# Performance work log

Hardware: AMD Instinct MI355X
Metric: run time of the kernel (lower is better)

## Reference

```python
import jax, jax.numpy as jnp
import numpy as np

B, S, H = 2, 2048, 1024
G, HEADS = 4, 16
HPG = HEADS // G          # heads per group = 4
HD = H // HEADS           # head_dim = 64
DG = H // G               # per-group proj dim = 256
SCALE = 1.0 / np.sqrt(HD)


def setup_inputs() -> dict:
    key = jax.random.key(0)
    ks = jax.random.split(key, 6)
    w = 0.02
    return {
        "hidden_states": jax.random.normal(ks[0], (B, S, H), dtype=jnp.float32),
        "Wq": jax.random.normal(ks[1], (G, DG, H), dtype=jnp.float32) * w,
        "bq": jnp.zeros((G, DG), dtype=jnp.float32),
        "Wk": jax.random.normal(ks[2], (G, DG, H), dtype=jnp.float32) * w,
        "bk": jnp.zeros((G, DG), dtype=jnp.float32),
        "Wv": jax.random.normal(ks[3], (G, DG, H), dtype=jnp.float32) * w,
        "bv": jnp.zeros((G, DG), dtype=jnp.float32),
        "Wo": jax.random.normal(ks[4], (H, H), dtype=jnp.float32) * w,
        "bo": jnp.zeros((H,), dtype=jnp.float32),
    }


def _proj_split(x, W, b):
    # x: [B,S,H], W: [G,DG,H], b: [G,DG] -> [B,G,HPG,S,HD]
    y = jnp.einsum("bsh,gdh->bgsd", x, W) + b[None, :, None, :]
    y = y.reshape(x.shape[0], G, x.shape[1], HPG, HD)
    return jnp.transpose(y, (0, 1, 3, 2, 4))


def reference(hidden_states, Wq, bq, Wk, bk, Wv, bv, Wo, bo):
    q = _proj_split(hidden_states, Wq, bq)  # [B,G,HPG,S,HD]
    k = _proj_split(hidden_states, Wk, bk)
    v = _proj_split(hidden_states, Wv, bv)
    scores = jnp.einsum("bghqd,bghkd->bghqk", q, k) * SCALE
    attn = jax.nn.softmax(scores.astype(jnp.float32), axis=-1).astype(v.dtype)
    ctx = jnp.einsum("bghqk,bghkd->bghqd", attn, v)  # [B,G,HPG,S,HD]
    # merge: heads ordered group-major, matching torch cat over group dim
    ctx = jnp.transpose(ctx, (0, 3, 1, 2, 4)).reshape(hidden_states.shape[0], hidden_states.shape[1], H)
    return jnp.einsum("bsh,oh->bso", ctx, Wo) + bo
```

## Files before the change

### kernel.cpp

```cpp
#include <hip/hip_runtime.h>

typedef __bf16 bf16x8 __attribute__((ext_vector_type(8)));
typedef __bf16 bf16x4 __attribute__((ext_vector_type(4)));
typedef short short4v __attribute__((ext_vector_type(4)));
typedef float f32x4 __attribute__((ext_vector_type(4)));

#define LOG2E 1.4426950408889634f

static __device__ __forceinline__ unsigned short f2bf(float f) {
  union { float f; unsigned int u; } c; c.f = f;
  return (unsigned short)((c.u + 0x7fffu + ((c.u >> 16) & 1u)) >> 16);
}

static __device__ __forceinline__ void gload16(const void* g, void* l) {
  __builtin_amdgcn_global_load_lds(
      (const __attribute__((address_space(1))) void*)g,
      (__attribute__((address_space(3))) void*)l, 16, 0, 0);
}

static __device__ __forceinline__ float expfast(float x) {
#if __has_builtin(__builtin_amdgcn_exp2f)
  return __builtin_amdgcn_exp2f(x * LOG2E);
#else
  return exp2f(x * LOG2E);
#endif
}

#if __has_builtin(__builtin_amdgcn_mfma_f32_16x16x16bf16_1k)
#define MFMA16_FALLBACK 0
static __device__ __forceinline__ f32x4 mfma16(bf16x4 a, bf16x4 b, f32x4 c) {
  return __builtin_amdgcn_mfma_f32_16x16x16bf16_1k(
      __builtin_bit_cast(short4v, a), __builtin_bit_cast(short4v, b), c, 0, 0, 0);
}
#else
#define MFMA16_FALLBACK 1
static __device__ __forceinline__ f32x4 mfma16(bf16x4 a, bf16x4 b, f32x4 c) {
  f32x4 d;
  asm("s_nop 1\n\tv_mfma_f32_16x16x16_bf16 %0, %1, %2, %3"
      : "=v"(d) : "v"(a), "v"(b), "v"(c));
  return d;
}
#endif

__global__ void cvt_all(const float* __restrict__ x,
                        const float* __restrict__ Wq,
                        const float* __restrict__ Wk,
                        const float* __restrict__ Wv,
                        const float* __restrict__ Wo,
                        ushort4* __restrict__ dst) {
  int i = blockIdx.x * 256 + threadIdx.x;
  const float* src;
  int off;
  if (i < 1048576) {
    src = x; off = i;
  } else {
    int t = (i - 1048576) >> 18;
    off = (i - 1048576) & 262143;
    src = (t == 0) ? Wq : (t == 1) ? Wk : (t == 2) ? Wv : Wo;
  }
  float4 f = ((const float4*)src)[off];
  ushort4 o;
  o.x = f2bf(f.x); o.y = f2bf(f.y); o.z = f2bf(f.z); o.w = f2bf(f.w);
  dst[i] = o;
}

__launch_bounds__(256, 2)
__global__ void qkv_gemm(const unsigned short* __restrict__ xb,
                         const unsigned short* __restrict__ wq,
                         const unsigned short* __restrict__ wk,
                         const unsigned short* __restrict__ wv,
                         const float* __restrict__ bq,
                         const float* __restrict__ bk,
                         const float* __restrict__ bv,
                         unsigned short* __restrict__ Qo,
                         unsigned short* __restrict__ Ko,
                         unsigned short* __restrict__ VTo) {
  __shared__ unsigned short As[128 * 32];
  __shared__ unsigned short Bs[128 * 32];
  const int s0 = blockIdx.x * 128;
  const int n0g = blockIdx.y * 128;
  const int qkv = n0g >> 10;
  const int d0 = n0g & 1023;
  const unsigned short* W = (qkv == 0) ? wq : ((qkv == 1) ? wk : wv);
  const float* bias = (qkv == 0) ? bq : ((qkv == 1) ? bk : bv);

  const unsigned short* Aptr; const unsigned short* Bptr;
  int Aoff, Boff;
  if (qkv < 2) { Aptr = W;  Aoff = d0; Bptr = xb; Boff = s0; }
  else         { Aptr = xb; Aoff = s0; Bptr = W;  Boff = d0; }

  const int tid = threadIdx.x;
  const int lane = tid & 63;
  const int wid = tid >> 6;
  const int wm = (wid >> 1) * 64;
  const int wn = (wid & 1) * 64;
  const int lm = lane & 15;
  const int quad = lane >> 4;

  const int c0 = tid, c1 = 256 + tid;
  const int ar0 = c0 >> 2, aj0 = c0 & 3;
  const int ar1 = c1 >> 2, aj1 = c1 & 3;

  f32x4 acc[4][4] = {};

  for (int kk = 0; kk < 1024; kk += 32) {
    gload16(Aptr + (size_t)(Aoff + ar0) * 1024 + kk + aj0 * 8, As + c0 * 8);
    gload16(Aptr + (size_t)(Aoff + ar1) * 1024 + kk + aj1 * 8, As + c1 * 8);
    gload16(Bptr + (size_t)(Boff + ar0) * 1024 + kk + aj0 * 8, Bs + c0 * 8);
    gload16(Bptr + (size_t)(Boff + ar1) * 1024 + kk + aj1 * 8, Bs + c1 * 8);
    __syncthreads();
    bf16x8 af[4], bff[4];
#pragma unroll
    for (int mt = 0; mt < 4; ++mt)
      af[mt] = *(const bf16x8*)(As + (wm + mt * 16 + lm) * 32 + quad * 8);
#pragma unroll
    for (int nt = 0; nt < 4; ++nt)
      bff[nt] = *(const bf16x8*)(Bs + (wn + nt * 16 + lm) * 32 + quad * 8);
#pragma unroll
    for (int mt = 0; mt < 4; ++mt)
#pragma unroll
      for (int nt = 0; nt < 4; ++nt)
        acc[mt][nt] = __builtin_amdgcn_mfma_f32_16x16x32_bf16(
            af[mt], bff[nt], acc[mt][nt], 0, 0, 0);
    __syncthreads();
  }

  if (qkv < 2) {
    unsigned short* OUT = (qkv == 0) ? Qo : Ko;
    const float scale = (qkv == 0) ? 0.125f : 1.0f;
#pragma unroll
    for (int mt = 0; mt < 4; ++mt) {
      const int d = d0 + wm + mt * 16 + quad * 4;
      const int g = d >> 8, hpg = (d >> 6) & 3, hd = d & 63;
      const float4 bb = *(const float4*)(bias + d);
#pragma unroll
      for (int nt = 0; nt < 4; ++nt) {
        const int srow = s0 + wn + nt * 16 + lm;
        const int bidx = srow >> 11, s = srow & 2047;
        const int head = (bidx * 4 + g) * 4 + hpg;
        ushort4 o;
        o.x = f2bf((acc[mt][nt][0] + bb.x) * scale);
        o.y = f2bf((acc[mt][nt][1] + bb.y) * scale);
        o.z = f2bf((acc[mt][nt][2] + bb.z) * scale);
        o.w = f2bf((acc[mt][nt][3] + bb.w) * scale);
        *(ushort4*)(OUT + (size_t)head * 131072 + (size_t)s * 64 + hd) = o;
      }
    }
  } else {
#pragma unroll
    for (int nt = 0; nt < 4; ++nt) {
      const int d = d0 + wn + nt * 16 + lm;
      const int g = d >> 8, hpg = (d >> 6) & 3, hd = d & 63;
      const float bb = bias[d];
#pragma unroll
      for (int mt = 0; mt < 4; ++mt) {
        const int sbase = s0 + wm + mt * 16 + quad * 4;
        const int bidx = sbase >> 11, s = sbase & 2047;
        const int head = (bidx * 4 + g) * 4 + hpg;
        ushort4 o;
        o.x = f2bf(acc[mt][nt][0] + bb);
        o.y = f2bf(acc[mt][nt][1] + bb);
        o.z = f2bf(acc[mt][nt][2] + bb);
        o.w = f2bf(acc[mt][nt][3] + bb);
        *(ushort4*)(VTo + (size_t)head * 131072 + (size_t)hd * 2048 + s) = o;
      }
    }
  }
}

static __device__ __forceinline__ void stage_kv(
    const unsigned short* Kh, const unsigned short* Vh, int kv0,
    unsigned short* ksl, unsigned short* vsl, int tid) {
#pragma unroll
  for (int t = 0; t < 4; ++t) {
    int i = t * 256 + tid;
    int slab = i >> 9, kv = (i >> 2) & 127, tp = i & 3;
    int tc = tp ^ ((kv >> 1) & 3);
    gload16(Kh + (size_t)(kv0 + kv) * 64 + slab * 32 + tc * 8, ksl + (size_t)i * 8);
  }
#pragma unroll
  for (int t = 0; t < 4; ++t) {
    int i = t * 256 + tid;
    int hd = i >> 4, tp = i & 15;
    int tc = tp ^ ((hd >> 1) & 7);
    gload16(Vh + (size_t)hd * 2048 + kv0 + tc * 8, vsl + (size_t)i * 8);
  }
}

__launch_bounds__(256, 2)
__global__ void attn_kernel(const unsigned short* __restrict__ Q,
                            const unsigned short* __restrict__ K,
                            const unsigned short* __restrict__ VT,
                            unsigned short* __restrict__ ctx) {
  __shared__ unsigned short Ks[2][8192];
  __shared__ unsigned short Vs[2][8192];

  const int head = blockIdx.y;
  const int q0 = blockIdx.x * 128;
  const int b = head >> 4;
  const int colbase = (head & 15) * 64;

  const unsigned short* Kh = K + (size_t)head * 131072;
  const unsigned short* Vh = VT + (size_t)head * 131072;

  const int tid = threadIdx.x;
  const int lane = tid & 63;
  const int w = tid >> 6;
  const int lm = lane & 15;
  const int quad = lane >> 4;

  bf16x8 qf[2][2];
#pragma unroll
  for (int nt = 0; nt < 2; ++nt) {
    const size_t qrow = (size_t)(q0 + w * 32 + nt * 16 + lm);
#pragma unroll
    for (int c = 0; c < 2; ++c)
      qf[c][nt] = *(const bf16x8*)(Q + (size_t)head * 131072 + qrow * 64 +
                                   c * 32 + quad * 8);
  }

  stage_kv(Kh, Vh, 0, Ks[0], Vs[0], tid);
  __syncthreads();

  float psum[2] = {0.f, 0.f};
  f32x4 oacc[4][2] = {};
  const int kchunk = (quad ^ ((lm >> 1) & 3)) * 8;

  for (int it = 0; it < 16; ++it) {
    const int buf = it & 1;
    if (it < 15)
      stage_kv(Kh, Vh, (it + 1) * 128, Ks[buf ^ 1], Vs[buf ^ 1], tid);

    const unsigned short* kb = Ks[buf];
    const unsigned short* vb = Vs[buf];

#pragma unroll
    for (int mt = 0; mt < 8; ++mt) {
      f32x4 s0 = {}, s1 = {};
#pragma unroll
      for (int c = 0; c < 2; ++c) {
        bf16x8 kf = *(const bf16x8*)(kb + c * 4096 + (mt * 16 + lm) * 32 + kchunk);
        s0 = __builtin_amdgcn_mfma_f32_16x16x32_bf16(kf, qf[c][0], s0, 0, 0, 0);
        s1 = __builtin_amdgcn_mfma_f32_16x16x32_bf16(kf, qf[c][1], s1, 0, 0, 0);
      }
      bf16x4 pf[2];
#pragma unroll
      for (int nt = 0; nt < 2; ++nt) {
        const f32x4 s = nt ? s1 : s0;
        float e0 = expfast(s[0]), e1 = expfast(s[1]);
        float e2 = expfast(s[2]), e3 = expfast(s[3]);
        psum[nt] += (e0 + e1) + (e2 + e3);
        bf16x4 t;
        t[0] = (__bf16)e0; t[1] = (__bf16)e1; t[2] = (__bf16)e2; t[3] = (__bf16)e3;
        pf[nt] = t;
      }
#pragma unroll
      for (int hm = 0; hm < 4; ++hm) {
        bf16x4 vf = *(const bf16x4*)(vb + (hm * 16 + lm) * 128 +
                                     (((mt * 4 + quad) ^ (lm & 14)) * 4));
        oacc[hm][0] = mfma16(vf, pf[0], oacc[hm][0]);
        oacc[hm][1] = mfma16(vf, pf[1], oacc[hm][1]);
      }
    }
    __syncthreads();
  }

#if MFMA16_FALLBACK
  asm volatile("s_nop 7\n\ts_nop 7");
#endif
#pragma unroll
  for (int nt = 0; nt < 2; ++nt) {
    float p = psum[nt];
    p += __shfl_xor(p, 16, 64);
    p += __shfl_xor(p, 32, 64);
    const float inv = 1.0f / p;
    const size_t row = (size_t)(b * 2048 + q0 + w * 32 + nt * 16 + lm);
#pragma unroll
    for (int hm = 0; hm < 4; ++hm) {
      ushort4 o;
      o.x = f2bf(oacc[hm][nt][0] * inv);
      o.y = f2bf(oacc[hm][nt][1] * inv);
      o.z = f2bf(oacc[hm][nt][2] * inv);
      o.w = f2bf(oacc[hm][nt][3] * inv);
      *(ushort4*)(ctx + row * 1024 + colbase + hm * 16 + quad * 4) = o;
    }
  }
}

__launch_bounds__(256, 2)
__global__ void out_gemm(const unsigned short* __restrict__ A,
                         const unsigned short* __restrict__ Wb,
                         const float* __restrict__ bo,
                         float* __restrict__ out) {
  __shared__ unsigned short As[128 * 32];
  __shared__ unsigned short Bs[128 * 32];
  const int s0 = blockIdx.x * 128;
  const int o0 = blockIdx.y * 128;

  const int tid = threadIdx.x;
  const int lane = tid & 63;
  const int wid = tid >> 6;
  const int wm = (wid >> 1) * 64;
  const int wn = (wid & 1) * 64;
  const int lm = lane & 15;
  const int quad = lane >> 4;

  const int c0 = tid, c1 = 256 + tid;
  const int ar0 = c0 >> 2, aj0 = c0 & 3;
  const int ar1 = c1 >> 2, aj1 = c1 & 3;

  f32x4 acc[4][4] = {};

  for (int kk = 0; kk < 1024; kk += 32) {
    gload16(Wb + (size_t)(o0 + ar0) * 1024 + kk + aj0 * 8, As + c0 * 8);
    gload16(Wb + (size_t)(o0 + ar1) * 1024 + kk + aj1 * 8, As + c1 * 8);
    gload16(A + (size_t)(s0 + ar0) * 1024 + kk + aj0 * 8, Bs + c0 * 8);
    gload16(A + (size_t)(s0 + ar1) * 1024 + kk + aj1 * 8, Bs + c1 * 8);
    __syncthreads();
    bf16x8 af[4], bff[4];
#pragma unroll
    for (int mt = 0; mt < 4; ++mt)
      af[mt] = *(const bf16x8*)(As + (wm + mt * 16 + lm) * 32 + quad * 8);
#pragma unroll
    for (int nt = 0; nt < 4; ++nt)
      bff[nt] = *(const bf16x8*)(Bs + (wn + nt * 16 + lm) * 32 + quad * 8);
#pragma unroll
    for (int mt = 0; mt < 4; ++mt)
#pragma unroll
      for (int nt = 0; nt < 4; ++nt)
        acc[mt][nt] = __builtin_amdgcn_mfma_f32_16x16x32_bf16(
            af[mt], bff[nt], acc[mt][nt], 0, 0, 0);
    __syncthreads();
  }

#pragma unroll
  for (int mt = 0; mt < 4; ++mt) {
    const int o = o0 + wm + mt * 16 + quad * 4;
    const float4 bb = *(const float4*)(bo + o);
#pragma unroll
    for (int nt = 0; nt < 4; ++nt) {
      const int s = s0 + wn + nt * 16 + lm;
      float4 v;
      v.x = acc[mt][nt][0] + bb.x;
      v.y = acc[mt][nt][1] + bb.y;
      v.z = acc[mt][nt][2] + bb.z;
      v.w = acc[mt][nt][3] + bb.w;
      *(float4*)(out + (size_t)s * 1024 + o) = v;
    }
  }
}

extern "C" void kernel_launch(void* const* d_in, const int* in_sizes, int n_in,
                              void* d_out, int out_size, void* d_ws, size_t ws_size,
                              hipStream_t stream) {
  const float* x  = (const float*)d_in[0];
  const float* Wq = (const float*)d_in[1];
  const float* bq = (const float*)d_in[2];
  const float* Wk = (const float*)d_in[3];
  const float* bk = (const float*)d_in[4];
  const float* Wv = (const float*)d_in[5];
  const float* bv = (const float*)d_in[6];
  const float* Wo = (const float*)d_in[7];
  const float* bo = (const float*)d_in[8];
  float* out = (float*)d_out;

  char* ws = (char*)d_ws;
  unsigned short* xb  = (unsigned short*)(ws + 0);
  unsigned short* wqb = (unsigned short*)(ws + 8388608);
  unsigned short* wkb = (unsigned short*)(ws + 10485760);
  unsigned short* wvb = (unsigned short*)(ws + 12582912);
  unsigned short* wob = (unsigned short*)(ws + 14680064);
  unsigned short* Qb  = (unsigned short*)(ws + 16777216);
  unsigned short* Kb  = (unsigned short*)(ws + 25165824);
  unsigned short* VTb = (unsigned short*)(ws + 33554432);
  unsigned short* ctxb= (unsigned short*)(ws + 41943040);
  if (ws_size < 50331648) return;

  cvt_all<<<8192, 256, 0, stream>>>(x, Wq, Wk, Wv, Wo, (ushort4*)ws);
  qkv_gemm<<<dim3(32, 24), 256, 0, stream>>>(xb, wqb, wkb, wvb, bq, bk, bv,
                                             Qb, Kb, VTb);
  attn_kernel<<<dim3(16, 32), 256, 0, stream>>>(Qb, Kb, VTb, ctxb);
  out_gemm<<<dim3(32, 8), 256, 0, stream>>>(ctxb, wob, bo, out);
}
```

Before: 198.5 us.

## Deepen GEMM K-tile to 64 with XOR-swizzled LDS and smaller out_gemm tiles

Both projection GEMMs now stage a 64-wide K slice per iteration instead of 32, which halves the number of barrier pairs. Shared-memory rows are XOR-swizzled by row index so the 128-byte rows avoid LDS bank conflicts on the MFMA fragment reads. The output GEMM switches to 128x64 tiles with a doubled grid and launch bounds raised to 4 blocks per CU, to fill more CUs (the old grid had only 256 blocks). The cost is more LDS per block and lower per-block reuse in out_gemm.

```diff
diff --git a/kernel.cpp b/kernel.cpp
--- a/kernel.cpp
+++ b/kernel.cpp
@@ -75,8 +75,8 @@
                          unsigned short* __restrict__ Qo,
                          unsigned short* __restrict__ Ko,
                          unsigned short* __restrict__ VTo) {
-  __shared__ unsigned short As[128 * 32];
-  __shared__ unsigned short Bs[128 * 32];
+  __shared__ unsigned short As[128 * 64];
+  __shared__ unsigned short Bs[128 * 64];
   const int s0 = blockIdx.x * 128;
   const int n0g = blockIdx.y * 128;
   const int qkv = n0g >> 10;
@@ -97,31 +97,40 @@
   const int lm = lane & 15;
   const int quad = lane >> 4;
 
-  const int c0 = tid, c1 = 256 + tid;
-  const int ar0 = c0 >> 2, aj0 = c0 & 3;
-  const int ar1 = c1 >> 2, aj1 = c1 & 3;
-
   f32x4 acc[4][4] = {};
 
-  for (int kk = 0; kk < 1024; kk += 32) {
-    gload16(Aptr + (size_t)(Aoff + ar0) * 1024 + kk + aj0 * 8, As + c0 * 8);
-    gload16(Aptr + (size_t)(Aoff + ar1) * 1024 + kk + aj1 * 8, As + c1 * 8);
-    gload16(Bptr + (size_t)(Boff + ar0) * 1024 + kk + aj0 * 8, Bs + c0 * 8);
-    gload16(Bptr + (size_t)(Boff + ar1) * 1024 + kk + aj1 * 8, Bs + c1 * 8);
+  for (int kk = 0; kk < 1024; kk += 64) {
+#pragma unroll
+    for (int t = 0; t < 4; ++t) {
+      int i = t * 256 + tid;
+      int row = i >> 3, tp = i & 7;
+      int seg = tp ^ (row & 7);
+      gload16(Aptr + (size_t)(Aoff + row) * 1024 + kk + seg * 8,
+              As + (size_t)i * 8);
+      gload16(Bptr + (size_t)(Boff + row) * 1024 + kk + seg * 8,
+              Bs + (size_t)i * 8);
+    }
     __syncthreads();
-    bf16x8 af[4], bff[4];
-#pragma unroll
-    for (int mt = 0; mt < 4; ++mt)
-      af[mt] = *(const bf16x8*)(As + (wm + mt * 16 + lm) * 32 + quad * 8);
-#pragma unroll
-    for (int nt = 0; nt < 4; ++nt)
-      bff[nt] = *(const bf16x8*)(Bs + (wn + nt * 16 + lm) * 32 + quad * 8);
-#pragma unroll
-    for (int mt = 0; mt < 4; ++mt)
-#pragma unroll
-      for (int nt = 0; nt < 4; ++nt)
-        acc[mt][nt] = __builtin_amdgcn_mfma_f32_16x16x32_bf16(
-            af[mt], bff[nt], acc[mt][nt], 0, 0, 0);
+#pragma unroll
+    for (int h = 0; h < 2; ++h) {
+      bf16x8 af[4], bff[4];
+#pragma unroll
+      for (int mt = 0; mt < 4; ++mt) {
+        int r = wm + mt * 16 + lm;
+        af[mt] = *(const bf16x8*)(As + r * 64 + (((h * 4 + quad) ^ (r & 7)) * 8));
+      }
+#pragma unroll
+      for (int nt = 0; nt < 4; ++nt) {
+        int r = wn + nt * 16 + lm;
+        bff[nt] = *(const bf16x8*)(Bs + r * 64 + (((h * 4 + quad) ^ (r & 7)) * 8));
+      }
+#pragma unroll
+      for (int mt = 0; mt < 4; ++mt)
+#pragma unroll
+        for (int nt = 0; nt < 4; ++nt)
+          acc[mt][nt] = __builtin_amdgcn_mfma_f32_16x16x32_bf16(
+              af[mt], bff[nt], acc[mt][nt], 0, 0, 0);
+    }
     __syncthreads();
   }
 
@@ -287,49 +296,62 @@
   }
 }
 
-__launch_bounds__(256, 2)
+__launch_bounds__(256, 4)
 __global__ void out_gemm(const unsigned short* __restrict__ A,
                          const unsigned short* __restrict__ Wb,
                          const float* __restrict__ bo,
                          float* __restrict__ out) {
-  __shared__ unsigned short As[128 * 32];
-  __shared__ unsigned short Bs[128 * 32];
-  const int s0 = blockIdx.x * 128;
+  __shared__ unsigned short As[128 * 64];
+  __shared__ unsigned short Bs[64 * 64];
+  const int s0 = blockIdx.x * 64;
   const int o0 = blockIdx.y * 128;
 
   const int tid = threadIdx.x;
   const int lane = tid & 63;
   const int wid = tid >> 6;
   const int wm = (wid >> 1) * 64;
-  const int wn = (wid & 1) * 64;
+  const int wn = (wid & 1) * 32;
   const int lm = lane & 15;
   const int quad = lane >> 4;
 
-  const int c0 = tid, c1 = 256 + tid;
-  const int ar0 = c0 >> 2, aj0 = c0 & 3;
-  const int ar1 = c1 >> 2, aj1 = c1 & 3;
-
-  f32x4 acc[4][4] = {};
-
-  for (int kk = 0; kk < 1024; kk += 32) {
-    gload16(Wb + (size_t)(o0 + ar0) * 1024 + kk + aj0 * 8, As + c0 * 8);
-    gload16(Wb + (size_t)(o0 + ar1) * 1024 + kk + aj1 * 8, As + c1 * 8);
-    gload16(A + (size_t)(s0 + ar0) * 1024 + kk + aj0 * 8, Bs + c0 * 8);
-    gload16(A + (size_t)(s0 + ar1) * 1024 + kk + aj1 * 8, Bs + c1 * 8);
+  f32x4 acc[4][2] = {};
+
+  for (int kk = 0; kk < 1024; kk += 64) {
+#pragma unroll
+    for (int t = 0; t < 4; ++t) {
+      int i = t * 256 + tid;
+      int row = i >> 3, tp = i & 7;
+      int seg = tp ^ (row & 7);
+      gload16(Wb + (size_t)(o0 + row) * 1024 + kk + seg * 8, As + (size_t)i * 8);
+    }
+#pragma unroll
+    for (int t = 0; t < 2; ++t) {
+      int i = t * 256 + tid;
+      int row = i >> 3, tp = i & 7;
+      int seg = tp ^ (row & 7);
+      gload16(A + (size_t)(s0 + row) * 1024 + kk + seg * 8, Bs + (size_t)i * 8);
+    }
     __syncthreads();
-    bf16x8 af[4], bff[4];
-#pragma unroll
-    for (int mt = 0; mt < 4; ++mt)
-      af[mt] = *(const bf16x8*)(As + (wm + mt * 16 + lm) * 32 + quad * 8);
-#pragma unroll
-    for (int nt = 0; nt < 4; ++nt)
-      bff[nt] = *(const bf16x8*)(Bs + (wn + nt * 16 + lm) * 32 + quad * 8);
-#pragma unroll
-    for (int mt = 0; mt < 4; ++mt)
-#pragma unroll
-      for (int nt = 0; nt < 4; ++nt)
-        acc[mt][nt] = __builtin_amdgcn_mfma_f32_16x16x32_bf16(
-            af[mt], bff[nt], acc[mt][nt], 0, 0, 0);
+#pragma unroll
+    for (int h = 0; h < 2; ++h) {
+      bf16x8 af[4], bff[2];
+#pragma unroll
+      for (int mt = 0; mt < 4; ++mt) {
+        int r = wm + mt * 16 + lm;
+        af[mt] = *(const bf16x8*)(As + r * 64 + (((h * 4 + quad) ^ (r & 7)) * 8));
+      }
+#pragma unroll
+      for (int nt = 0; nt < 2; ++nt) {
+        int r = wn + nt * 16 + lm;
+        bff[nt] = *(const bf16x8*)(Bs + r * 64 + (((h * 4 + quad) ^ (r & 7)) * 8));
+      }
+#pragma unroll
+      for (int mt = 0; mt < 4; ++mt)
+#pragma unroll
+        for (int nt = 0; nt < 2; ++nt)
+          acc[mt][nt] = __builtin_amdgcn_mfma_f32_16x16x32_bf16(
+              af[mt], bff[nt], acc[mt][nt], 0, 0, 0);
+    }
     __syncthreads();
   }
 
@@ -338,7 +360,7 @@
     const int o = o0 + wm + mt * 16 + quad * 4;
     const float4 bb = *(const float4*)(bo + o);
 #pragma unroll
-    for (int nt = 0; nt < 4; ++nt) {
+    for (int nt = 0; nt < 2; ++nt) {
       const int s = s0 + wn + nt * 16 + lm;
       float4 v;
       v.x = acc[mt][nt][0] + bb.x;
@@ -380,5 +402,5 @@
   qkv_gemm<<<dim3(32, 24), 256, 0, stream>>>(xb, wqb, wkb, wvb, bq, bk, bv,
                                              Qb, Kb, VTb);
   attn_kernel<<<dim3(16, 32), 256, 0, stream>>>(Qb, Kb, VTb, ctxb);
-  out_gemm<<<dim3(32, 8), 256, 0, stream>>>(ctxb, wob, bo, out);
-}
+  out_gemm<<<dim3(64, 8), 256, 0, stream>>>(ctxb, wob, bo, out);
+}
```

Measured after the change: 197.0 us. About the same (-0.7%).
